# Optimization experiments

Measured on AMD Instinct MI355X. Metric: run time of the kernel, lower is better.

## Reference

```python
import jax, jax.numpy as jnp
import numpy as np

N = 50000
E = 800000
F_IN = 128


def _gat(h, src, dst, W, a_src, a_dst, bias, heads, out_ch, concat):
    n = h.shape[0]
    z = (h @ W.T).reshape(n, heads, out_ch)              # [N,H,C]
    alpha_s = jnp.sum(z * a_src, axis=-1)                # [N,H]
    alpha_d = jnp.sum(z * a_dst, axis=-1)                # [N,H]
    logits = jax.nn.leaky_relu(alpha_s[src] + alpha_d[dst], 0.2)  # [Etot,H]
    m = jax.ops.segment_max(logits, dst, num_segments=n)
    ex = jnp.exp(logits - m[dst])
    denom = jax.ops.segment_sum(ex, dst, num_segments=n)
    w = ex / (denom[dst] + 1e-16)                        # [Etot,H]
    agg = jax.ops.segment_sum(w[:, :, None] * z[src], dst, num_segments=n)  # [N,H,C]
    if concat:
        out = agg.reshape(n, heads * out_ch)
    else:
        out = agg.mean(axis=1)
    return out + bias


def setup_inputs() -> dict:
    key = jax.random.key(0)
    ks = jax.random.split(key, 16)
    s = lambda *sh: 1.0 / np.sqrt(sh[-1])
    inp = {
        "x": jax.random.normal(ks[0], (N, F_IN), jnp.float32),
        "edge_index": jax.random.randint(ks[1], (2, E), 0, N, jnp.int64),
        # GraphConv(no_node_features=128 -> 128, aggr='add')
        "W_rel": jax.random.normal(ks[2], (128, F_IN), jnp.float32) * s(128, F_IN),
        "b_rel": jnp.zeros((128,), jnp.float32),
        "W_root": jax.random.normal(ks[3], (128, F_IN), jnp.float32) * s(128, F_IN),
        # GATConv(128 -> 8, heads=8, concat) => 64
        "W1": jax.random.normal(ks[4], (64, 128), jnp.float32) * s(64, 128),
        "a1_src": jax.random.normal(ks[5], (8, 8), jnp.float32) * 0.35,
        "a1_dst": jax.random.normal(ks[6], (8, 8), jnp.float32) * 0.35,
        "b1": jnp.zeros((64,), jnp.float32),
        # GATConv(64 -> 64, heads=1, concat=False)
        "W2": jax.random.normal(ks[7], (64, 64), jnp.float32) * s(64, 64),
        "a2_src": jax.random.normal(ks[8], (1, 64), jnp.float32) * 0.125,
        "a2_dst": jax.random.normal(ks[9], (1, 64), jnp.float32) * 0.125,
        "b2": jnp.zeros((64,), jnp.float32),
        "Wr": jax.random.normal(ks[10], (1, 64), jnp.float32) * s(1, 64),
        "br": jnp.zeros((1,), jnp.float32),
    }
    return inp


def reference(x, edge_index, W_rel, b_rel, W_root, W1, a1_src, a1_dst, b1,
              W2, a2_src, a2_dst, b2, Wr, br):
    src, dst = edge_index[0], edge_index[1]
    # GraphConv, aggr='add': W_rel @ sum_{j in N(i)} x_j + b + W_root @ x_i
    nbr = jax.ops.segment_sum(x[src], dst, num_segments=N)
    h = nbr @ W_rel.T + b_rel + x @ W_root.T
    h = jax.nn.elu(h)
    # GATConv adds self-loops by default
    loop = jnp.arange(N, dtype=edge_index.dtype)
    src2 = jnp.concatenate([src, loop])
    dst2 = jnp.concatenate([dst, loop])
    h = _gat(h, src2, dst2, W1, a1_src, a1_dst, b1, heads=8, out_ch=8, concat=True)
    h = jax.nn.elu(h)
    h = _gat(h, src2, dst2, W2, a2_src, a2_dst, b2, heads=1, out_ch=64, concat=False)
    # final 'mean' aggregation over all nodes (single graph)
    g = jnp.mean(h, axis=0, keepdims=True)               # [1,64]
    return g @ Wr.T + br                                  # [1,1]
```

## Files before the change

kernel.cpp:

```cpp
#include <hip/hip_runtime.h>
#include <hip/hip_bf16.h>
#include <math.h>

#define N_NODES 50000
#define N_EDGES 800000
#define F_IN 128
#define NBUCK 391
#define EPB 4096
#define NBB 196
#define CAP 4096

typedef __attribute__((ext_vector_type(8))) short bf16x8;
typedef __attribute__((ext_vector_type(4))) float f32x4;
typedef __attribute__((ext_vector_type(2))) float f32x2;
typedef unsigned long long ull;

__device__ __forceinline__ float elu_f(float x)   { return x > 0.f ? x : expm1f(x); }
__device__ __forceinline__ float lrelu_f(float x) { return x > 0.f ? x : 0.2f * x; }
__device__ __forceinline__ int   clampN(int v)    { return v < 0 ? 0 : (v >= N_NODES ? N_NODES - 1 : v); }
__device__ __forceinline__ float bits2f(unsigned int u) { union { unsigned int u; float f; } x; x.u = u; return x.f; }
__device__ __forceinline__ float bf2f(unsigned short s) { return bits2f(((unsigned int)s) << 16); }
__device__ __forceinline__ unsigned short f2bfbits(float f) {
    __hip_bfloat16 b = __float2bfloat16(f);
    return __builtin_bit_cast(unsigned short, b);
}
__device__ __forceinline__ unsigned int pack2(float lo, float hi) {
    return ((unsigned int)f2bfbits(hi) << 16) | f2bfbits(lo);
}

#define CAST_X_IDS (N_NODES * 32)
#define CAST_IDS (CAST_X_IDS + 32768 + 8192 + 4096)
#define CASTB ((CAST_IDS + 255) / 256)
__global__ __launch_bounds__(256) void k_prep(const float* __restrict__ x,
                                              const float* __restrict__ W_rel,
                                              const float* __restrict__ W_root,
                                              const float* __restrict__ W1,
                                              const float* __restrict__ W2,
                                              __hip_bfloat16* __restrict__ Abuf,
                                              unsigned int* __restrict__ x8,
                                              __hip_bfloat16* __restrict__ Wc,
                                              __hip_bfloat16* __restrict__ W1b,
                                              __hip_bfloat16* __restrict__ W2b,
                                              int* __restrict__ gcount,
                                              float* __restrict__ red,
                                              int* __restrict__ done) {
    int tid = threadIdx.x;
    if (blockIdx.x == 0) {
        red[tid] = 0.f;
        if (tid < NBUCK) gcount[tid] = 0;
        if (tid + 256 < NBUCK) gcount[tid + 256] = 0;
        if (tid == 0) done[0] = 0;
    }
    int id = blockIdx.x * 256 + tid;
    if (id < CAST_X_IDS) {
        int i = id >> 5, c4 = (id & 31) * 4;
        float4 v = *(const float4*)&x[(size_t)i * 128 + c4];
        ull p = (ull)f2bfbits(v.x) | ((ull)f2bfbits(v.y) << 16)
              | ((ull)f2bfbits(v.z) << 32) | ((ull)f2bfbits(v.w) << 48);
        *(ull*)&Abuf[(size_t)i * 256 + 128 + c4] = p;
        int t = __builtin_amdgcn_cvt_pk_fp8_f32(v.x, v.y, 0, false);
        t = __builtin_amdgcn_cvt_pk_fp8_f32(v.z, v.w, t, true);
        x8[(size_t)i * 32 + (id & 31)] = (unsigned int)t;
    } else if (id < CAST_IDS) {
        int j = id - CAST_X_IDS;
        if (j < 32768) {
            int cc = j >> 8, k = j & 255;
            float v = (k < 128) ? W_rel[cc * 128 + k] : W_root[cc * 128 + (k - 128)];
            Wc[j] = __float2bfloat16(v);
        } else if (j < 32768 + 8192) {
            W1b[j - 32768] = __float2bfloat16(W1[j - 32768]);
        } else {
            W2b[j - 32768 - 8192] = __float2bfloat16(W2[j - 32768 - 8192]);
        }
    }
}

__global__ __launch_bounds__(256) void k_bscatter(const int* __restrict__ src,
                                                  const int* __restrict__ dst,
                                                  int* __restrict__ gcount,
                                                  unsigned int* __restrict__ ebuf) {
    __shared__ int hist[NBUCK];
    __shared__ int hbase[NBUCK];
    int tid = threadIdx.x;
    for (int j = tid; j < NBUCK; j += 256) hist[j] = 0;
    __syncthreads();
    int base = blockIdx.x * EPB;
    unsigned int myP[EPB / 256]; int myB[EPB / 256], myR[EPB / 256];
    #pragma unroll
    for (int t = 0; t < EPB / 256; ++t) {
        int e = base + t * 256 + tid;
        if (e < N_EDGES) {
            int d = clampN(dst[e]);
            int s = clampN(src[e]);
            myP[t] = ((unsigned int)s << 7) | (unsigned int)(d & 127);
            myB[t] = d >> 7;
            myR[t] = atomicAdd(&hist[d >> 7], 1);
        } else myB[t] = -1;
    }
    __syncthreads();
    for (int j = tid; j < NBUCK; j += 256)
        if (hist[j]) hbase[j] = j * CAP + atomicAdd(&gcount[j], hist[j]);
    __syncthreads();
    #pragma unroll
    for (int t = 0; t < EPB / 256; ++t) {
        if (myB[t] >= 0) ebuf[hbase[myB[t]] + myR[t]] = myP[t];
    }
}

__global__ __launch_bounds__(256) void k_bfinal(const unsigned int* __restrict__ ebuf,
                                                const int* __restrict__ gcount,
                                                int2* __restrict__ offs,
                                                int* __restrict__ csr) {
    __shared__ int cnt[128];
    __shared__ int cur[128];
    __shared__ int ws[4];
    int b = blockIdx.x;
    int tid = threadIdx.x;
    int node0 = b << 7;
    int k0 = b * CAP, k1 = k0 + gcount[b];
    if (tid < 128) cnt[tid] = 0;
    __syncthreads();
    for (int k = k0 + tid; k < k1; k += 256)
        atomicAdd(&cnt[ebuf[k] & 127u], 1);
    __syncthreads();
    int lane = tid & 63;
    int v = (tid < 128) ? cnt[tid] : 0;
    int x = v;
    #pragma unroll
    for (int d = 1; d < 64; d <<= 1) {
        int t = __shfl_up(x, d, 64);
        if (lane >= d) x += t;
    }
    if (lane == 63) ws[tid >> 6] = x;
    __syncthreads();
    if (tid < 128) {
        int add = (tid >> 6) ? ws[0] : 0;
        int excl = k0 + add + x - v;
        cur[tid] = excl;
        int node = node0 + tid;
        if (node < N_NODES) offs[node] = make_int2(excl, excl + v);
    }
    __syncthreads();
    for (int k = k0 + tid; k < k1; k += 256) {
        unsigned int e = ebuf[k];
        int r = atomicAdd(&cur[e & 127u], 1);
        csr[r] = (int)(e >> 7);
    }
}

__global__ __launch_bounds__(256) void k_gather(const unsigned int* __restrict__ x8,
                                                const int2* __restrict__ offs,
                                                const int* __restrict__ csr,
                                                ull* __restrict__ outNbr) {
    int i = blockIdx.x * 8 + (threadIdx.x >> 5);
    int l = threadIdx.x & 31;
    int2 oe = offs[i];
    int k0 = oe.x, k1 = oe.y;
    float a0 = 0.f, a1 = 0.f, a2 = 0.f, a3 = 0.f;
    for (int kb = k0; kb < k1; kb += 8) {
        int s[8]; int vm[8];
        #pragma unroll
        for (int j = 0; j < 8; ++j) {
            int kk = kb + j;
            vm[j] = kk < k1;
            s[j] = csr[vm[j] ? kk : k1 - 1];
        }
        unsigned int u[8];
        #pragma unroll
        for (int j = 0; j < 8; ++j) u[j] = x8[(size_t)s[j] * 32 + l];
        #pragma unroll
        for (int j = 0; j < 8; ++j) {
            if (vm[j]) {
                f32x2 lo = __builtin_amdgcn_cvt_pk_f32_fp8(u[j], false);
                f32x2 hi = __builtin_amdgcn_cvt_pk_f32_fp8(u[j], true);
                a0 += lo.x; a1 += lo.y; a2 += hi.x; a3 += hi.y;
            }
        }
    }
    outNbr[(size_t)i * 64 + l] = (ull)pack2(a0, a1) | ((ull)pack2(a2, a3) << 32);
}

__global__ __launch_bounds__(256) void k_gemm12(const __hip_bfloat16* __restrict__ A,
                                                const __hip_bfloat16* __restrict__ Wc,
                                                const float* __restrict__ bias,
                                                const __hip_bfloat16* __restrict__ W1b,
                                                const float* __restrict__ a_src,
                                                const float* __restrict__ a_dst,
                                                float* __restrict__ as_o,
                                                float* __restrict__ ad_o,
                                                unsigned int* __restrict__ z8) {
    __shared__ __align__(16) short smem[64 * 136];
    short (*sA)[40] = (short(*)[40])smem;
    short (*sW)[40] = (short(*)[40])(smem + 64 * 40);
    int tid = threadIdx.x;
    int lane = tid & 63, wave = tid >> 6;
    int quad = lane >> 4, l16 = lane & 15;
    int node0 = blockIdx.x * 64;
    int srow = tid >> 2, schk = (tid & 3) * 8;
    int ga = node0 + srow; if (ga >= N_NODES) ga = N_NODES - 1;
    const short* Ap = (const short*)A + (size_t)ga * 256 + schk;
    const short* Wp = (const short*)Wc;
    f32x4 acc[8];
    #pragma unroll
    for (int t = 0; t < 8; ++t) acc[t] = (f32x4){0.f, 0.f, 0.f, 0.f};
    for (int k0 = 0; k0 < 256; k0 += 32) {
        *(bf16x8*)&sA[srow][schk] = *(const bf16x8*)(Ap + k0);
        #pragma unroll
        for (int it = 0; it < 2; ++it) {
            int wrow = srow + it * 64;
            *(bf16x8*)&sW[wrow][schk] = *(const bf16x8*)(Wp + (size_t)wrow * 256 + k0 + schk);
        }
        __syncthreads();
        bf16x8 a = *(const bf16x8*)&sA[wave * 16 + l16][quad * 8];
        #pragma unroll
        for (int nt = 0; nt < 8; ++nt) {
            bf16x8 b = *(const bf16x8*)&sW[nt * 16 + l16][quad * 8];
            acc[nt] = __builtin_amdgcn_mfma_f32_16x16x32_bf16(a, b, acc[nt], 0, 0, 0);
        }
        __syncthreads();
    }
    #pragma unroll
    for (int nt = 0; nt < 8; ++nt) {
        int col = nt * 16 + l16;
        float bv = bias[col];
        #pragma unroll
        for (int r = 0; r < 4; ++r) {
            int row = wave * 16 + quad * 4 + r;
            smem[row * 136 + col] = (short)f2bfbits(elu_f(acc[nt][r] + bv));
        }
    }
    __syncthreads();
    f32x4 acc2[4];
    #pragma unroll
    for (int t = 0; t < 4; ++t) acc2[t] = (f32x4){0.f, 0.f, 0.f, 0.f};
    const short* W1p = (const short*)W1b;
    #pragma unroll
    for (int k0 = 0; k0 < 128; k0 += 32) {
        bf16x8 a = *(const bf16x8*)&smem[(wave * 16 + l16) * 136 + k0 + quad * 8];
        #pragma unroll
        for (int nt = 0; nt < 4; ++nt) {
            bf16x8 b = *(const bf16x8*)(W1p + (size_t)(nt * 16 + l16) * 128 + k0 + quad * 8);
            acc2[nt] = __builtin_amdgcn_mfma_f32_16x16x32_bf16(a, b, acc2[nt], 0, 0, 0);
        }
    }
    __syncthreads();
    #pragma unroll
    for (int nt = 0; nt < 4; ++nt) {
        int col = nt * 16 + l16;
        #pragma unroll
        for (int r = 0; r < 4; ++r) {
            int row = wave * 16 + quad * 4 + r;
            smem[row * 72 + col] = (short)f2bfbits(acc2[nt][r]);
        }
    }
    __syncthreads();
    int row = tid >> 2, chunk = tid & 3;
    int gi = node0 + row;
    float v[16];
    bf16x8 c0 = *(const bf16x8*)&smem[row * 72 + chunk * 16];
    bf16x8 c1 = *(const bf16x8*)&smem[row * 72 + chunk * 16 + 8];
    #pragma unroll
    for (int j = 0; j < 8; ++j) {
        v[j]     = bf2f((unsigned short)c0[j]);
        v[8 + j] = bf2f((unsigned short)c1[j]);
    }
    float ps0 = 0.f, pd0 = 0.f, ps1 = 0.f, pd1 = 0.f;
    #pragma unroll
    for (int j = 0; j < 8; ++j) {
        ps0 += v[j] * a_src[chunk * 16 + j];
        pd0 += v[j] * a_dst[chunk * 16 + j];
        ps1 += v[8 + j] * a_src[chunk * 16 + 8 + j];
        pd1 += v[8 + j] * a_dst[chunk * 16 + 8 + j];
    }
    if (gi < N_NODES) {
        as_o[(size_t)gi * 8 + 2 * chunk]     = ps0;
        as_o[(size_t)gi * 8 + 2 * chunk + 1] = ps1;
        ad_o[(size_t)gi * 8 + 2 * chunk]     = pd0;
        ad_o[(size_t)gi * 8 + 2 * chunk + 1] = pd1;
        #pragma unroll
        for (int wi = 0; wi < 4; ++wi) {
            int t = __builtin_amdgcn_cvt_pk_fp8_f32(v[4 * wi], v[4 * wi + 1], 0, false);
            t = __builtin_amdgcn_cvt_pk_fp8_f32(v[4 * wi + 2], v[4 * wi + 3], t, true);
            z8[(size_t)gi * 16 + chunk * 4 + wi] = (unsigned int)t;
        }
    }
}

__global__ __launch_bounds__(256) void k_gat1z2(const unsigned int* __restrict__ z8,
                                                const float* __restrict__ as1,
                                                const float* __restrict__ ad1,
                                                const float* __restrict__ b1,
                                                const int2* __restrict__ offs,
                                                const int* __restrict__ csr,
                                                const __hip_bfloat16* __restrict__ W2b,
                                                const float* __restrict__ a2s,
                                                const float* __restrict__ a2d,
                                                const float* __restrict__ Wr,
                                                float* __restrict__ as2,
                                                float* __restrict__ ad2,
                                                float* __restrict__ zr) {
    __shared__ __align__(16) short sH2[16 * 72];
    __shared__ __align__(16) short sZ2[16 * 72];
    int iloc = threadIdx.x >> 4;
    int i = blockIdx.x * 16 + iloc;
    int l = threadIdx.x & 15;
    int hd = l >> 1;
    int wh = l & 7, slot = l >> 3;
    int2 oe = offs[i];
    int k0 = oe.x, k1 = oe.y;
    float ad_h = ad1[(size_t)i * 8 + hd];
    float adw  = ad1[(size_t)i * 8 + wh];
    float e_self = __expf(lrelu_f(as1[(size_t)i * 8 + hd] + ad_h));
    unsigned int uz = z8[(size_t)i * 16 + l];
    f32x2 zlo = __builtin_amdgcn_cvt_pk_f32_fp8(uz, false);
    f32x2 zhi = __builtin_amdgcn_cvt_pk_f32_fp8(uz, true);
    float acc0 = e_self * zlo.x, acc1 = e_self * zlo.y;
    float acc2 = e_self * zhi.x, acc3 = e_self * zhi.y;
    float denp = 0.f;
    for (int kb = k0; kb < k1; kb += 8) {
        int sr[4]; float er[4];
        #pragma unroll
        for (int m = 0; m < 4; ++m) {
            int kk = kb + 2 * m + slot;
            bool v = kk < k1;
            int s = csr[v ? kk : k1 - 1];
            sr[m] = s;
            er[m] = v ? __expf(lrelu_f(as1[(size_t)s * 8 + wh] + adw)) : 0.f;
            denp += er[m];
        }
        int sj[8]; float ej[8]; unsigned int u[8];
        #pragma unroll
        for (int m = 0; m < 4; ++m) {
            #pragma unroll
            for (int sb = 0; sb < 2; ++sb) {
                sj[2 * m + sb] = __shfl(sr[m], sb * 8 + hd, 16);
                ej[2 * m + sb] = __shfl(er[m], sb * 8 + hd, 16);
            }
        }
        #pragma unroll
        for (int j = 0; j < 8; ++j) u[j] = z8[(size_t)sj[j] * 16 + l];
        #pragma unroll
        for (int j = 0; j < 8; ++j) {
            f32x2 alo = __builtin_amdgcn_cvt_pk_f32_fp8(u[j], false);
            f32x2 ahi = __builtin_amdgcn_cvt_pk_f32_fp8(u[j], true);
            acc0 += ej[j] * alo.x; acc1 += ej[j] * alo.y;
            acc2 += ej[j] * ahi.x; acc3 += ej[j] * ahi.y;
        }
    }
    denp += __shfl_xor(denp, 8, 16);
    float den = __shfl(denp, hd, 16) + e_self;
    float inv = 1.f / den;
    float r0 = elu_f(acc0 * inv + b1[4 * l + 0]);
    float r1 = elu_f(acc1 * inv + b1[4 * l + 1]);
    float r2 = elu_f(acc2 * inv + b1[4 * l + 2]);
    float r3 = elu_f(acc3 * inv + b1[4 * l + 3]);
    *(ull*)&sH2[iloc * 72 + 4 * l] = (ull)pack2(r0, r1) | ((ull)pack2(r2, r3) << 32);
    __syncthreads();
    int lane = threadIdx.x & 63, wave = threadIdx.x >> 6;
    int quad = lane >> 4, l16 = lane & 15;
    f32x4 accz = (f32x4){0.f, 0.f, 0.f, 0.f};
    const short* W2p = (const short*)W2b;
    #pragma unroll
    for (int kk0 = 0; kk0 < 64; kk0 += 32) {
        bf16x8 a = *(const bf16x8*)&sH2[l16 * 72 + kk0 + quad * 8];
        bf16x8 b = *(const bf16x8*)(W2p + (size_t)(wave * 16 + l16) * 64 + kk0 + quad * 8);
        accz = __builtin_amdgcn_mfma_f32_16x16x32_bf16(a, b, accz, 0, 0, 0);
    }
    #pragma unroll
    for (int r = 0; r < 4; ++r)
        sZ2[(quad * 4 + r) * 72 + wave * 16 + l16] = (short)f2bfbits(accz[r]);
    __syncthreads();
    ull pz = *(const ull*)&sZ2[iloc * 72 + 4 * l];
    float v0 = bf2f((unsigned short)(pz & 0xffff));
    float v1 = bf2f((unsigned short)((pz >> 16) & 0xffff));
    float v2 = bf2f((unsigned short)((pz >> 32) & 0xffff));
    float v3 = bf2f((unsigned short)(pz >> 48));
    float ps = v0 * a2s[4 * l + 0] + v1 * a2s[4 * l + 1] + v2 * a2s[4 * l + 2] + v3 * a2s[4 * l + 3];
    float pd = v0 * a2d[4 * l + 0] + v1 * a2d[4 * l + 1] + v2 * a2d[4 * l + 2] + v3 * a2d[4 * l + 3];
    float pr = v0 * Wr[4 * l + 0]  + v1 * Wr[4 * l + 1]  + v2 * Wr[4 * l + 2]  + v3 * Wr[4 * l + 3];
    #pragma unroll
    for (int d = 8; d >= 1; d >>= 1) {
        ps += __shfl_xor(ps, d, 16);
        pd += __shfl_xor(pd, d, 16);
        pr += __shfl_xor(pr, d, 16);
    }
    if (l == 0) { as2[i] = ps; ad2[i] = pd; zr[i] = pr; }
}

__global__ __launch_bounds__(256) void k_gat2s(const float* __restrict__ zr,
                                               const float* __restrict__ as2,
                                               const float* __restrict__ ad2,
                                               const int2* __restrict__ offs,
                                               const int* __restrict__ csr,
                                               const float* __restrict__ b2,
                                               const float* __restrict__ Wr,
                                               const float* __restrict__ br,
                                               float* __restrict__ red,
                                               int* __restrict__ done,
                                               float* __restrict__ out) {
    __shared__ float wsum[4];
    __shared__ int lastFlag;
    int tid = threadIdx.x;
    int n = blockIdx.x * 64 + (tid >> 2);
    int r = tid & 3;
    float c = 0.f;
    if (n < N_NODES) {
        int2 oe = offs[n];
        float ad = ad2[n];
        float den = 0.f, num = 0.f;
        for (int k = oe.x + r; k < oe.y; k += 4) {
            int s = csr[k];
            float e = __expf(lrelu_f(as2[s] + ad));
            den += e;
            num += e * zr[s];
        }
        den += __shfl_xor(den, 1, 64); den += __shfl_xor(den, 2, 64);
        num += __shfl_xor(num, 1, 64); num += __shfl_xor(num, 2, 64);
        if (r == 0) {
            float es = __expf(lrelu_f(as2[n] + ad));
            den += es;
            num += es * zr[n];
            c = num / den;
        }
    }
    #pragma unroll
    for (int d = 4; d <= 32; d <<= 1) c += __shfl_xor(c, d, 64);
    int lane = tid & 63, wave = tid >> 6;
    if (lane == 0) wsum[wave] = c;
    __syncthreads();
    if (tid == 0) {
        float s = wsum[0] + wsum[1] + wsum[2] + wsum[3];
        atomicAdd(&red[blockIdx.x & 255], s);
        __threadfence();
        int old = atomicAdd(done, 1);
        lastFlag = (old == (int)gridDim.x - 1);
    }
    __syncthreads();
    if (lastFlag) {
        __threadfence();
        if (tid < 64) {
            float rv = atomicAdd(&red[tid], 0.f) + atomicAdd(&red[tid + 64], 0.f)
                     + atomicAdd(&red[tid + 128], 0.f) + atomicAdd(&red[tid + 192], 0.f);
            float p = rv * (1.0f / N_NODES) + b2[tid] * Wr[tid];
            #pragma unroll
            for (int d = 32; d >= 1; d >>= 1) p += __shfl_xor(p, d, 64);
            if (tid == 0) out[0] = p + br[0];
        }
    }
}

extern "C" void kernel_launch(void* const* d_in, const int* in_sizes, int n_in,
                              void* d_out, int out_size, void* d_ws, size_t ws_size,
                              hipStream_t stream) {
    const float* x      = (const float*)d_in[0];
    const int*   edges  = (const int*)d_in[1];
    const float* W_rel  = (const float*)d_in[2];
    const float* b_rel  = (const float*)d_in[3];
    const float* W_root = (const float*)d_in[4];
    const float* W1     = (const float*)d_in[5];
    const float* a1s    = (const float*)d_in[6];
    const float* a1d    = (const float*)d_in[7];
    const float* b1     = (const float*)d_in[8];
    const float* W2     = (const float*)d_in[9];
    const float* a2s    = (const float*)d_in[10];
    const float* a2d    = (const float*)d_in[11];
    const float* b2     = (const float*)d_in[12];
    const float* Wr     = (const float*)d_in[13];
    const float* br     = (const float*)d_in[14];
    float* out = (float*)d_out;

    const int* src = edges;
    const int* dst = edges + N_EDGES;

    char* ws = (char*)d_ws;
    size_t p = 0;
    auto alloc = [&](size_t bytes) -> void* {
        void* r = ws + p;
        p = (p + bytes + 255) & ~(size_t)255;
        return r;
    };
    unsigned int* ebuf = (unsigned int*)alloc((size_t)NBUCK * CAP * 4);
    int2*  offs    = (int2*)alloc((size_t)N_NODES * 8);
    int*   csr     = (int*)alloc((size_t)NBUCK * CAP * 4);
    int*   gcount  = (int*)alloc((size_t)NBUCK * 4);
    __hip_bfloat16* Abuf = (__hip_bfloat16*)alloc((size_t)N_NODES * 256 * 2);
    unsigned int* x8 = (unsigned int*)alloc((size_t)N_NODES * 32 * 4);
    __hip_bfloat16* Wc   = (__hip_bfloat16*)alloc((size_t)128 * 256 * 2);
    __hip_bfloat16* W1b  = (__hip_bfloat16*)alloc((size_t)64 * 128 * 2);
    __hip_bfloat16* W2b  = (__hip_bfloat16*)alloc((size_t)64 * 64 * 2);
    float* as1 = (float*)alloc((size_t)N_NODES * 8 * 4);
    float* ad1 = (float*)alloc((size_t)N_NODES * 8 * 4);
    float* as2 = (float*)alloc((size_t)N_NODES * 4);
    float* ad2 = (float*)alloc((size_t)N_NODES * 4);
    float* zr  = (float*)alloc((size_t)N_NODES * 4);
    unsigned int* z1e8 = (unsigned int*)alloc((size_t)N_NODES * 16 * 4);
    float* red = (float*)alloc(256 * 4);
    int*   done = (int*)alloc(4);

    const int MB   = (N_NODES + 63) / 64;
    const int NB8  = N_NODES / 8;
    const int NB16 = N_NODES / 16;

    k_prep    <<<CASTB, 256, 0, stream>>>(x, W_rel, W_root, W1, W2,
                                          Abuf, x8, Wc, W1b, W2b, gcount, red, done);
    k_bscatter<<<NBB, 256, 0, stream>>>(src, dst, gcount, ebuf);
    k_bfinal  <<<NBUCK, 256, 0, stream>>>(ebuf, gcount, offs, csr);
    k_gather  <<<NB8, 256, 0, stream>>>(x8, offs, csr, (ull*)Abuf);
    k_gemm12  <<<MB, 256, 0, stream>>>(Abuf, Wc, b_rel, W1b, a1s, a1d, as1, ad1, z1e8);
    k_gat1z2  <<<NB16, 256, 0, stream>>>(z1e8, as1, ad1, b1, offs, csr,
                                         W2b, a2s, a2d, Wr, as2, ad2, zr);
    k_gat2s   <<<MB, 256, 0, stream>>>(zr, as2, ad2, offs, csr, b2, Wr, br,
                                       red, done, out);
}
```

Measured before the change: 223.2 us.

## Merge edge bucket scatter into prep kernel and pack GAT2 node scalars

The edge bucket scatter and the feature/weight casting now run as disjoint block ranges of a single launch. The zeroing of counters moves into a tiny separate kernel so the merged kernel's atomics start from a cleared state, which keeps the launch count the same but lets the scatter and cast work overlap on the device. Separately, the GAT2 source attention scalar and the projected value are packed into one float2 array, so each gathered edge in the second attention layer makes one 8-byte load instead of two scattered 4-byte loads.

```diff
diff --git a/kernel.cpp b/kernel.cpp
--- a/kernel.cpp
+++ b/kernel.cpp
@@ -28,82 +28,79 @@
     return ((unsigned int)f2bfbits(hi) << 16) | f2bfbits(lo);
 }
 
+#define ZINTS (NBUCK + 256 + 1)
+__global__ __launch_bounds__(256) void k_zero(int* __restrict__ zbuf) {
+    int id = blockIdx.x * 256 + threadIdx.x;
+    if (id < ZINTS) zbuf[id] = 0;
+}
+
 #define CAST_X_IDS (N_NODES * 32)
 #define CAST_IDS (CAST_X_IDS + 32768 + 8192 + 4096)
 #define CASTB ((CAST_IDS + 255) / 256)
-__global__ __launch_bounds__(256) void k_prep(const float* __restrict__ x,
+__global__ __launch_bounds__(256) void k_prep(const int* __restrict__ src,
+                                              const int* __restrict__ dst,
+                                              const float* __restrict__ x,
                                               const float* __restrict__ W_rel,
                                               const float* __restrict__ W_root,
                                               const float* __restrict__ W1,
                                               const float* __restrict__ W2,
+                                              int* __restrict__ gcount,
+                                              unsigned int* __restrict__ ebuf,
                                               __hip_bfloat16* __restrict__ Abuf,
                                               unsigned int* __restrict__ x8,
                                               __hip_bfloat16* __restrict__ Wc,
                                               __hip_bfloat16* __restrict__ W1b,
-                                              __hip_bfloat16* __restrict__ W2b,
-                                              int* __restrict__ gcount,
-                                              float* __restrict__ red,
-                                              int* __restrict__ done) {
-    int tid = threadIdx.x;
-    if (blockIdx.x == 0) {
-        red[tid] = 0.f;
-        if (tid < NBUCK) gcount[tid] = 0;
-        if (tid + 256 < NBUCK) gcount[tid + 256] = 0;
-        if (tid == 0) done[0] = 0;
-    }
-    int id = blockIdx.x * 256 + tid;
-    if (id < CAST_X_IDS) {
-        int i = id >> 5, c4 = (id & 31) * 4;
-        float4 v = *(const float4*)&x[(size_t)i * 128 + c4];
-        ull p = (ull)f2bfbits(v.x) | ((ull)f2bfbits(v.y) << 16)
-              | ((ull)f2bfbits(v.z) << 32) | ((ull)f2bfbits(v.w) << 48);
-        *(ull*)&Abuf[(size_t)i * 256 + 128 + c4] = p;
-        int t = __builtin_amdgcn_cvt_pk_fp8_f32(v.x, v.y, 0, false);
-        t = __builtin_amdgcn_cvt_pk_fp8_f32(v.z, v.w, t, true);
-        x8[(size_t)i * 32 + (id & 31)] = (unsigned int)t;
-    } else if (id < CAST_IDS) {
-        int j = id - CAST_X_IDS;
-        if (j < 32768) {
-            int cc = j >> 8, k = j & 255;
-            float v = (k < 128) ? W_rel[cc * 128 + k] : W_root[cc * 128 + (k - 128)];
-            Wc[j] = __float2bfloat16(v);
-        } else if (j < 32768 + 8192) {
-            W1b[j - 32768] = __float2bfloat16(W1[j - 32768]);
-        } else {
-            W2b[j - 32768 - 8192] = __float2bfloat16(W2[j - 32768 - 8192]);
-        }
-    }
-}
-
-__global__ __launch_bounds__(256) void k_bscatter(const int* __restrict__ src,
-                                                  const int* __restrict__ dst,
-                                                  int* __restrict__ gcount,
-                                                  unsigned int* __restrict__ ebuf) {
+                                              __hip_bfloat16* __restrict__ W2b) {
     __shared__ int hist[NBUCK];
     __shared__ int hbase[NBUCK];
     int tid = threadIdx.x;
-    for (int j = tid; j < NBUCK; j += 256) hist[j] = 0;
-    __syncthreads();
-    int base = blockIdx.x * EPB;
-    unsigned int myP[EPB / 256]; int myB[EPB / 256], myR[EPB / 256];
-    #pragma unroll
-    for (int t = 0; t < EPB / 256; ++t) {
-        int e = base + t * 256 + tid;
-        if (e < N_EDGES) {
-            int d = clampN(dst[e]);
-            int s = clampN(src[e]);
-            myP[t] = ((unsigned int)s << 7) | (unsigned int)(d & 127);
-            myB[t] = d >> 7;
-            myR[t] = atomicAdd(&hist[d >> 7], 1);
-        } else myB[t] = -1;
-    }
-    __syncthreads();
-    for (int j = tid; j < NBUCK; j += 256)
-        if (hist[j]) hbase[j] = j * CAP + atomicAdd(&gcount[j], hist[j]);
-    __syncthreads();
-    #pragma unroll
-    for (int t = 0; t < EPB / 256; ++t) {
-        if (myB[t] >= 0) ebuf[hbase[myB[t]] + myR[t]] = myP[t];
+    if (blockIdx.x < NBB) {
+        for (int j = tid; j < NBUCK; j += 256) hist[j] = 0;
+        __syncthreads();
+        int base = blockIdx.x * EPB;
+        unsigned int myP[EPB / 256]; int myB[EPB / 256], myR[EPB / 256];
+        #pragma unroll
+        for (int t = 0; t < EPB / 256; ++t) {
+            int e = base + t * 256 + tid;
+            if (e < N_EDGES) {
+                int d = clampN(dst[e]);
+                int s = clampN(src[e]);
+                myP[t] = ((unsigned int)s << 7) | (unsigned int)(d & 127);
+                myB[t] = d >> 7;
+                myR[t] = atomicAdd(&hist[d >> 7], 1);
+            } else myB[t] = -1;
+        }
+        __syncthreads();
+        for (int j = tid; j < NBUCK; j += 256)
+            if (hist[j]) hbase[j] = j * CAP + atomicAdd(&gcount[j], hist[j]);
+        __syncthreads();
+        #pragma unroll
+        for (int t = 0; t < EPB / 256; ++t) {
+            if (myB[t] >= 0) ebuf[hbase[myB[t]] + myR[t]] = myP[t];
+        }
+    } else {
+        int id = (blockIdx.x - NBB) * 256 + tid;
+        if (id < CAST_X_IDS) {
+            int i = id >> 5, c4 = (id & 31) * 4;
+            float4 v = *(const float4*)&x[(size_t)i * 128 + c4];
+            ull p = (ull)f2bfbits(v.x) | ((ull)f2bfbits(v.y) << 16)
+                  | ((ull)f2bfbits(v.z) << 32) | ((ull)f2bfbits(v.w) << 48);
+            *(ull*)&Abuf[(size_t)i * 256 + 128 + c4] = p;
+            int t = __builtin_amdgcn_cvt_pk_fp8_f32(v.x, v.y, 0, false);
+            t = __builtin_amdgcn_cvt_pk_fp8_f32(v.z, v.w, t, true);
+            x8[(size_t)i * 32 + (id & 31)] = (unsigned int)t;
+        } else if (id < CAST_IDS) {
+            int j = id - CAST_X_IDS;
+            if (j < 32768) {
+                int cc = j >> 8, k = j & 255;
+                float v = (k < 128) ? W_rel[cc * 128 + k] : W_root[cc * 128 + (k - 128)];
+                Wc[j] = __float2bfloat16(v);
+            } else if (j < 32768 + 8192) {
+                W1b[j - 32768] = __float2bfloat16(W1[j - 32768]);
+            } else {
+                W2b[j - 32768 - 8192] = __float2bfloat16(W2[j - 32768 - 8192]);
+            }
+        }
     }
 }
 
@@ -296,9 +293,8 @@
                                                 const float* __restrict__ a2s,
                                                 const float* __restrict__ a2d,
                                                 const float* __restrict__ Wr,
-                                                float* __restrict__ as2,
-                                                float* __restrict__ ad2,
-                                                float* __restrict__ zr) {
+                                                float2* __restrict__ az,
+                                                float* __restrict__ ad2) {
     __shared__ __align__(16) short sH2[16 * 72];
     __shared__ __align__(16) short sZ2[16 * 72];
     int iloc = threadIdx.x >> 4;
@@ -384,11 +380,10 @@
         pd += __shfl_xor(pd, d, 16);
         pr += __shfl_xor(pr, d, 16);
     }
-    if (l == 0) { as2[i] = ps; ad2[i] = pd; zr[i] = pr; }
-}
-
-__global__ __launch_bounds__(256) void k_gat2s(const float* __restrict__ zr,
-                                               const float* __restrict__ as2,
+    if (l == 0) { az[i] = make_float2(ps, pr); ad2[i] = pd; }
+}
+
+__global__ __launch_bounds__(256) void k_gat2s(const float2* __restrict__ az,
                                                const float* __restrict__ ad2,
                                                const int2* __restrict__ offs,
                                                const int* __restrict__ csr,
@@ -410,16 +405,18 @@
         float den = 0.f, num = 0.f;
         for (int k = oe.x + r; k < oe.y; k += 4) {
             int s = csr[k];
-            float e = __expf(lrelu_f(as2[s] + ad));
+            float2 a_z = az[s];
+            float e = __expf(lrelu_f(a_z.x + ad));
             den += e;
-            num += e * zr[s];
+            num += e * a_z.y;
         }
         den += __shfl_xor(den, 1, 64); den += __shfl_xor(den, 2, 64);
         num += __shfl_xor(num, 1, 64); num += __shfl_xor(num, 2, 64);
         if (r == 0) {
-            float es = __expf(lrelu_f(as2[n] + ad));
+            float2 self = az[n];
+            float es = __expf(lrelu_f(self.x + ad));
             den += es;
-            num += es * zr[n];
+            num += es * self.y;
             c = num / den;
         }
     }
@@ -479,10 +476,14 @@
         p = (p + bytes + 255) & ~(size_t)255;
         return r;
     };
+    int* zbuf = (int*)alloc((size_t)ZINTS * 4);
+    int*   gcount = zbuf;
+    float* red    = (float*)(zbuf + NBUCK);
+    int*   done   = zbuf + NBUCK + 256;
+
     unsigned int* ebuf = (unsigned int*)alloc((size_t)NBUCK * CAP * 4);
     int2*  offs    = (int2*)alloc((size_t)N_NODES * 8);
     int*   csr     = (int*)alloc((size_t)NBUCK * CAP * 4);
-    int*   gcount  = (int*)alloc((size_t)NBUCK * 4);
     __hip_bfloat16* Abuf = (__hip_bfloat16*)alloc((size_t)N_NODES * 256 * 2);
     unsigned int* x8 = (unsigned int*)alloc((size_t)N_NODES * 32 * 4);
     __hip_bfloat16* Wc   = (__hip_bfloat16*)alloc((size_t)128 * 256 * 2);
@@ -490,25 +491,22 @@
     __hip_bfloat16* W2b  = (__hip_bfloat16*)alloc((size_t)64 * 64 * 2);
     float* as1 = (float*)alloc((size_t)N_NODES * 8 * 4);
     float* ad1 = (float*)alloc((size_t)N_NODES * 8 * 4);
-    float* as2 = (float*)alloc((size_t)N_NODES * 4);
+    float2* az = (float2*)alloc((size_t)N_NODES * 8);
     float* ad2 = (float*)alloc((size_t)N_NODES * 4);
-    float* zr  = (float*)alloc((size_t)N_NODES * 4);
     unsigned int* z1e8 = (unsigned int*)alloc((size_t)N_NODES * 16 * 4);
-    float* red = (float*)alloc(256 * 4);
-    int*   done = (int*)alloc(4);
 
     const int MB   = (N_NODES + 63) / 64;
     const int NB8  = N_NODES / 8;
     const int NB16 = N_NODES / 16;
 
-    k_prep    <<<CASTB, 256, 0, stream>>>(x, W_rel, W_root, W1, W2,
-                                          Abuf, x8, Wc, W1b, W2b, gcount, red, done);
-    k_bscatter<<<NBB, 256, 0, stream>>>(src, dst, gcount, ebuf);
+    k_zero    <<<(ZINTS + 255) / 256, 256, 0, stream>>>(zbuf);
+    k_prep    <<<NBB + CASTB, 256, 0, stream>>>(src, dst, x, W_rel, W_root, W1, W2,
+                                                gcount, ebuf, Abuf, x8, Wc, W1b, W2b);
     k_bfinal  <<<NBUCK, 256, 0, stream>>>(ebuf, gcount, offs, csr);
     k_gather  <<<NB8, 256, 0, stream>>>(x8, offs, csr, (ull*)Abuf);
     k_gemm12  <<<MB, 256, 0, stream>>>(Abuf, Wc, b_rel, W1b, a1s, a1d, as1, ad1, z1e8);
     k_gat1z2  <<<NB16, 256, 0, stream>>>(z1e8, as1, ad1, b1, offs, csr,
-                                         W2b, a2s, a2d, Wr, as2, ad2, zr);
-    k_gat2s   <<<MB, 256, 0, stream>>>(zr, as2, ad2, offs, csr, b2, Wr, br,
+                                         W2b, a2s, a2d, Wr, az, ad2);
+    k_gat2s   <<<MB, 256, 0, stream>>>(az, ad2, offs, csr, b2, Wr, br,
                                        red, done, out);
 }
```

Measured after the change: 216.9 us. -2.8%, faster.
